# Performance work log

Hardware: AMD Instinct MI355X
Metric: run time of the kernel (lower is better)

The kernel has to match this reference:

```python
import jax, jax.numpy as jnp
import numpy as np

B, N, E = 64, 64, 512          # batch, objects per image, edges per image
OBJ_DIM, Q_DIM, KS = 2048, 1024, 8
HID = Q_DIM // 2               # 512


def setup_inputs() -> dict:
    key = jax.random.key(0)
    k1, k2, k3, k4, k5, k6 = jax.random.split(key, 6)
    node_feats = jax.random.normal(k1, (B, N, OBJ_DIM), jnp.float32)
    q_feats = jax.random.normal(k2, (B, Q_DIM), jnp.float32)
    # Edges: per-image random (i, j) pairs with self-loops removed, indices into
    # the flattened [B*N*N] pairwise tensor, sorted by batch (m//b per image).
    i = jax.random.randint(k3, (B, E), 0, N)
    off = jax.random.randint(k4, (B, E), 1, N)
    j = (i + off) % N
    base = jnp.arange(B)[:, None] * (N * N)
    indexes = (base + i * N + j).reshape(-1).astype(jnp.int32)  # [B*E]
    scale = 0.02
    W_obj = jax.random.normal(k5, (OBJ_DIM, HID), jnp.float32) * scale
    b_obj = jnp.zeros((HID,), jnp.float32)
    W_q = jax.random.normal(k6, (Q_DIM, HID * KS), jnp.float32) * scale
    b_q = jnp.zeros((HID * KS,), jnp.float32)
    return {"node_feats": node_feats, "q_feats": q_feats, "indexes": indexes,
            "W_obj": W_obj, "b_obj": b_obj, "W_q": W_q, "b_q": b_q}


def reference(node_feats, q_feats, indexes, W_obj, b_obj, W_q, b_q):
    b, n, _ = node_feats.shape
    # obj_prob_l: Linear + ReLU -> [B, N, HID]
    node_h = jax.nn.relu(jnp.einsum('bno,oh->bnh', node_feats, W_obj) + b_obj)
    hid = node_h.shape[-1]
    # node_intersect(method='sum') then gather via graph.indexes:
    # equivalent to gathering (i, j) pairs directly instead of materializing [B*N*N, HID]
    bidx = indexes // (n * n)
    rem = indexes % (n * n)
    src = rem // n
    dst = rem % n
    obj_e = node_h[bidx, src] + node_h[bidx, dst]            # [M, HID]
    # q_prob_l: Linear + ReLU -> [B, HID*KS], viewed as per-edge kernels [M, HID, KS]
    q_h = jax.nn.relu(q_feats @ W_q + b_q)                   # [B, HID*KS]
    ks = q_h.shape[-1] // hid
    q_e = q_h.reshape(b, hid, ks)[bidx]                      # [M, HID, KS]
    # batched (1,HID) @ (HID,KS) dot product, then divide by per-kernel norm
    edge_logit = jnp.einsum('mh,mhk->mk', obj_e, q_e)        # [M, KS]
    edge_logit = edge_logit / jnp.linalg.norm(q_e, axis=1)   # [M, KS]
    return edge_logit
```

## Files before the change

### kernel.cpp

```cpp
#include <hip/hip_runtime.h>
#include <hip/hip_bf16.h>


using bf16x8 = __attribute__((ext_vector_type(8))) __bf16;
using f32x4  = __attribute__((ext_vector_type(4))) float;

__device__ __forceinline__ unsigned short f2bf(float f) {
    unsigned int u = __float_as_uint(f);
    unsigned int r = (u + 0x7FFFu + ((u >> 16) & 1u)) >> 16;
    return (unsigned short)r;
}

__device__ __forceinline__ uint4 pk8u(f32x4 a, f32x4 b) {
    union { unsigned short us[8]; uint4 u4; } r;
    r.us[0] = f2bf(a[0]); r.us[1] = f2bf(a[1]); r.us[2] = f2bf(a[2]); r.us[3] = f2bf(a[3]);
    r.us[4] = f2bf(b[0]); r.us[5] = f2bf(b[1]); r.us[6] = f2bf(b[2]); r.us[7] = f2bf(b[3]);
    return r.u4;
}

__device__ __forceinline__ bf16x8 pk8(f32x4 a, f32x4 b) {
    union { uint4 u4; bf16x8 v; } r;
    r.u4 = pk8u(a, b);
    return r.v;
}

__device__ __forceinline__ void gl_lds16(const void* g, void* l) {
    __builtin_amdgcn_global_load_lds(
        (const __attribute__((address_space(1))) unsigned int*)g,
        (__attribute__((address_space(3))) unsigned int*)l,
        16, 0, 0);
}

__global__ __launch_bounds__(256) void cvt_k(const float* __restrict__ nf,
                                             const float* __restrict__ W,
                                             unsigned short* __restrict__ A,
                                             unsigned short* __restrict__ WT) {
    __shared__ float lds[32][33];
    int bid = blockIdx.x;
    if (bid < 2048) {
        int tid = bid * 256 + threadIdx.x;
        for (int p = tid; p < 1048576; p += 524288) {
            int r = p >> 8;
            int grp = p & 255;
            int chunk = grp >> 3, slot = grp & 7;
            int sslot = slot ^ (r & 7);
            const float* src = nf + (size_t)r * 2048 + chunk * 64 + sslot * 8;
            f32x4 v0 = *(const f32x4*)(src);
            f32x4 v1 = *(const f32x4*)(src + 4);
            *(uint4*)(A + (size_t)r * 2048 + chunk * 64 + slot * 8) = pk8u(v0, v1);
        }
    } else {
        int g = bid - 2048;
        int k0 = (g & 63) * 32, n0 = (g >> 6) * 32;
        int tx = threadIdx.x & 31, ty = threadIdx.x >> 5;
#pragma unroll
        for (int j = 0; j < 4; ++j)
            lds[ty + j * 8][tx] = W[(size_t)(k0 + ty + j * 8) * 512 + n0 + tx];
        __syncthreads();
#pragma unroll
        for (int j = 0; j < 4; ++j) {
            int n = n0 + ty + j * 8;
            int k = k0 + tx;
            int chunk = k >> 6, off = k & 63;
            int ksw = chunk * 64 + (((off >> 3) ^ (n & 7)) << 3) + (k & 7);
            WT[(size_t)n * 2048 + ksw] = f2bf(lds[tx][ty + j * 8]);
        }
    }
}

__device__ __forceinline__ void gemm1_body(char* smem, int g1, int t,
                                           const unsigned short* __restrict__ A,
                                           const unsigned short* __restrict__ BT,
                                           const float* __restrict__ bias,
                                           float* __restrict__ C) {
    unsigned short* AsmB = (unsigned short*)smem;
    unsigned short* BsmB = (unsigned short*)(smem + 16384);

    int swz = (g1 & 7) * 64 + (g1 >> 3);
    int by = swz >> 3, bx = swz & 7;
    int m0 = by * 64, n0 = bx * 64;

    int lane = t & 63, w = t >> 6;
    int wm = w >> 1, wn = w & 1;
    int l15 = lane & 15, l16 = lane >> 4;

    const unsigned short* aG = A  + (size_t)(m0 + w * 16 + (lane >> 3)) * 2048 + (lane & 7) * 8;
    const unsigned short* bG = BT + (size_t)(n0 + w * 16 + (lane >> 3)) * 2048 + (lane & 7) * 8;

    f32x4 acc[2][2];
#pragma unroll
    for (int i = 0; i < 2; ++i)
#pragma unroll
        for (int j = 0; j < 2; ++j) acc[i][j] = (f32x4){0.f, 0.f, 0.f, 0.f};

#define G1_STAGE(buf, step)                                                    \
    do {                                                                       \
        int _ko = (step) * 64;                                                 \
        unsigned short* _aL = AsmB + (buf) * 4096 + (w * 16) * 64;             \
        unsigned short* _bL = BsmB + (buf) * 4096 + (w * 16) * 64;             \
        gl_lds16(aG + _ko, _aL);                                               \
        gl_lds16(aG + (size_t)8 * 2048 + _ko, _aL + 512);                      \
        gl_lds16(bG + _ko, _bL);                                               \
        gl_lds16(bG + (size_t)8 * 2048 + _ko, _bL + 512);                      \
    } while (0)

    G1_STAGE(0, 0);
    __syncthreads();

    for (int s = 0; s < 32; ++s) {
        int cur = s & 1;
        if (s < 31) G1_STAGE(cur ^ 1, s + 1);

        const char* Ab = (const char*)(AsmB + cur * 4096);
        const char* Bb = (const char*)(BsmB + cur * 4096);
        int r0 = wm * 32 + l15, r1 = r0 + 16;
        int c0n = wn * 32 + l15, c1n = c0n + 16;
#pragma unroll
        for (int ks = 0; ks < 2; ++ks) {
            int sx = ((ks * 4 + l16) ^ (l15 & 7)) << 4;
            bf16x8 a0 = *(const bf16x8*)(Ab + r0 * 128 + sx);
            bf16x8 a1 = *(const bf16x8*)(Ab + r1 * 128 + sx);
            bf16x8 b0 = *(const bf16x8*)(Bb + c0n * 128 + sx);
            bf16x8 b1 = *(const bf16x8*)(Bb + c1n * 128 + sx);
            acc[0][0] = __builtin_amdgcn_mfma_f32_16x16x32_bf16(a0, b0, acc[0][0], 0, 0, 0);
            acc[0][1] = __builtin_amdgcn_mfma_f32_16x16x32_bf16(a0, b1, acc[0][1], 0, 0, 0);
            acc[1][0] = __builtin_amdgcn_mfma_f32_16x16x32_bf16(a1, b0, acc[1][0], 0, 0, 0);
            acc[1][1] = __builtin_amdgcn_mfma_f32_16x16x32_bf16(a1, b1, acc[1][1], 0, 0, 0);
        }
        __syncthreads();
    }
#undef G1_STAGE

#pragma unroll
    for (int fm = 0; fm < 2; ++fm)
#pragma unroll
        for (int fn = 0; fn < 2; ++fn) {
            int col = n0 + wn * 32 + fn * 16 + l15;
            float bv = bias[col];
#pragma unroll
            for (int j = 0; j < 4; ++j) {
                int row = m0 + wm * 32 + fm * 16 + l16 * 4 + j;
                float v = acc[fm][fn][j] + bv;
                C[(size_t)row * 512 + col] = v > 0.f ? v : 0.f;
            }
        }
}

#define LDK2 136
__device__ __forceinline__ void gemm2_body(char* smem, int bid2, int t,
                                           const float* __restrict__ qf,
                                           const float* __restrict__ Wq,
                                           float* __restrict__ part) {
    auto Asm = reinterpret_cast<unsigned short(*)[LDK2]>(smem);
    auto Bsm = reinterpret_cast<unsigned short(*)[LDK2]>(smem + 64 * LDK2 * 2);

    int lane = t & 63, w = t >> 6;
    int l15 = lane & 15, l16 = lane >> 4;
    int c0 = (bid2 & 63) * 64;
    int k0 = (bid2 >> 6) * 128;

#pragma unroll
    for (int j = 0; j < 4; ++j) {
        int g = t + j * 256;
        int row = g >> 4, kc = g & 15;
        const float* src = qf + (size_t)row * 1024 + k0 + kc * 8;
        f32x4 v0 = *(const f32x4*)(src);
        f32x4 v1 = *(const f32x4*)(src + 4);
        *(uint4*)(&Asm[row][kc * 8]) = pk8u(v0, v1);
    }
    {
        int kg = t >> 4, cg = t & 15;
        f32x4 wv[8];
#pragma unroll
        for (int kk = 0; kk < 8; ++kk)
            wv[kk] = *(const f32x4*)(Wq + (size_t)(k0 + kg * 8 + kk) * 4096 + c0 + cg * 4);
#pragma unroll
        for (int cc = 0; cc < 4; ++cc) {
            union { unsigned short us[8]; uint4 u4; } p;
#pragma unroll
            for (int kk = 0; kk < 8; ++kk) p.us[kk] = f2bf(wv[kk][cc]);
            *(uint4*)(&Bsm[cg * 4 + cc][kg * 8]) = p.u4;
        }
    }
    __syncthreads();

    f32x4 acc[4];
#pragma unroll
    for (int i = 0; i < 4; ++i) acc[i] = (f32x4){0.f, 0.f, 0.f, 0.f};

#pragma unroll
    for (int ks = 0; ks < 4; ++ks) {
        bf16x8 bfr = *(const bf16x8*)(&Bsm[w * 16 + l15][ks * 32 + l16 * 8]);
#pragma unroll
        for (int i = 0; i < 4; ++i) {
            bf16x8 afr = *(const bf16x8*)(&Asm[i * 16 + l15][ks * 32 + l16 * 8]);
            acc[i] = __builtin_amdgcn_mfma_f32_16x16x32_bf16(afr, bfr, acc[i], 0, 0, 0);
        }
    }

    float* pz = part + (size_t)(bid2 >> 6) * 262144;
    int col = c0 + w * 16 + l15;
#pragma unroll
    for (int i = 0; i < 4; ++i)
#pragma unroll
        for (int j = 0; j < 4; ++j) {
            int row = i * 16 + l16 * 4 + j;
            pz[(size_t)row * 4096 + col] = acc[i][j];
        }
}

__global__ __launch_bounds__(256) void gemm_fused(const unsigned short* A,
                                                  const unsigned short* BT,
                                                  const float* bias, float* C,
                                                  const float* qf, const float* Wq,
                                                  float* part) {
    __shared__ __align__(16) char smem[34816];
    int bid = blockIdx.x, t = threadIdx.x;
    if (bid < 512) gemm1_body(smem, bid, t, A, BT, bias, C);
    else           gemm2_body(smem, bid - 512, t, qf, Wq, part);
}
__global__ __launch_bounds__(256) void gemm1_only(const unsigned short* A,
                                                  const unsigned short* BT,
                                                  const float* bias, float* C) {
    __shared__ __align__(16) char smem[34816];
    gemm1_body(smem, blockIdx.x, threadIdx.x, A, BT, bias, C);
}
__global__ __launch_bounds__(256) void gemm2_only(const float* qf, const float* Wq,
                                                  float* part) {
    __shared__ __align__(16) char smem[34816];
    gemm2_body(smem, blockIdx.x, threadIdx.x, qf, Wq, part);
}

__global__ __launch_bounds__(256) void tail_k(const float* __restrict__ part,
                                              const float* __restrict__ bq,
                                              const float* __restrict__ node_h,
                                              const int* __restrict__ idxs,
                                              float* __restrict__ out) {
    __shared__ float qs[4096];
    __shared__ float red[4][8];
    __shared__ float inv[8];
    __shared__ float Pl[64][8];

    int b = blockIdx.x, t = threadIdx.x;
    int lane = t & 63, w = t >> 6;
    int l15 = lane & 15, l16 = lane >> 4;

#pragma unroll
    for (int j = 0; j < 4; ++j) {
        int c = j * 1024 + t * 4;
        f32x4 a = (f32x4){0.f, 0.f, 0.f, 0.f};
#pragma unroll
        for (int z = 0; z < 8; ++z)
            a += *(const f32x4*)(part + (size_t)z * 262144 + (size_t)b * 4096 + c);
        f32x4 bb = *(const f32x4*)(bq + c);
#pragma unroll
        for (int i = 0; i < 4; ++i) {
            float v = a[i] + bb[i];
            a[i] = v > 0.f ? v : 0.f;
        }
        *(f32x4*)(&qs[c]) = a;
    }
    __syncthreads();

    {
        const float* row = qs + t * 16;
        float sq[8] = {0.f, 0.f, 0.f, 0.f, 0.f, 0.f, 0.f, 0.f};
#pragma unroll
        for (int j = 0; j < 4; ++j) {
            f32x4 v = *(const f32x4*)(row + j * 4);
            sq[(j * 4 + 0) & 7] += v[0] * v[0];
            sq[(j * 4 + 1) & 7] += v[1] * v[1];
            sq[(j * 4 + 2) & 7] += v[2] * v[2];
            sq[(j * 4 + 3) & 7] += v[3] * v[3];
        }
#pragma unroll
        for (int k = 0; k < 8; ++k) {
            float v = sq[k];
            v += __shfl_xor(v, 1);  v += __shfl_xor(v, 2);  v += __shfl_xor(v, 4);
            v += __shfl_xor(v, 8);  v += __shfl_xor(v, 16); v += __shfl_xor(v, 32);
            sq[k] = v;
        }
        if (lane == 0) {
#pragma unroll
            for (int k = 0; k < 8; ++k) red[w][k] = sq[k];
        }
    }
    __syncthreads();
    if (t < 8) {
        float s = red[0][t] + red[1][t] + red[2][t] + red[3][t];
        inv[t] = 1.0f / sqrtf(s);
    }
    __syncthreads();

    {
        bool active = l15 < 8;
        float invv = active ? inv[l15] : 0.f;
        const float* arow = node_h + (size_t)(b * 64 + w * 16 + l15) * 512 + l16 * 8;
        f32x4 acc = (f32x4){0.f, 0.f, 0.f, 0.f};
#pragma unroll
        for (int kt = 0; kt < 16; ++kt) {
            f32x4 v0 = *(const f32x4*)(arow + kt * 32);
            f32x4 v1 = *(const f32x4*)(arow + kt * 32 + 4);
            bf16x8 af = pk8(v0, v1);
            union { unsigned short us[8]; bf16x8 v; } bqf;
#pragma unroll
            for (int i = 0; i < 8; ++i)
                bqf.us[i] = active ? f2bf(qs[kt * 256 + (l16 * 8 + i) * 8 + l15]) : 0;
            acc = __builtin_amdgcn_mfma_f32_16x16x32_bf16(af, bqf.v, acc, 0, 0, 0);
        }
        if (active) {
#pragma unroll
            for (int j = 0; j < 4; ++j)
                Pl[w * 16 + l16 * 4 + j][l15] = acc[j] * invv;
        }
    }
    __syncthreads();

#pragma unroll
    for (int e = 0; e < 2; ++e) {
        int m = b * 512 + e * 256 + t;
        int idx = idxs[m];
        int r = idx & 4095;
        int src = r >> 6, dst = r & 63;
        f32x4 o0 = *(const f32x4*)(&Pl[src][0]) + *(const f32x4*)(&Pl[dst][0]);
        f32x4 o1 = *(const f32x4*)(&Pl[src][4]) + *(const f32x4*)(&Pl[dst][4]);
        *(f32x4*)(out + (size_t)m * 8)     = o0;
        *(f32x4*)(out + (size_t)m * 8 + 4) = o1;
    }
}

extern "C" void kernel_launch(void* const* d_in, const int* in_sizes, int n_in,
                              void* d_out, int out_size, void* d_ws, size_t ws_size,
                              hipStream_t stream) {
    const float* node_feats = (const float*)d_in[0];
    const float* q_feats    = (const float*)d_in[1];
    const int*   indexes    = (const int*)d_in[2];
    const float* W_obj      = (const float*)d_in[3];
    const float* b_obj      = (const float*)d_in[4];
    const float* W_q        = (const float*)d_in[5];
    const float* b_q        = (const float*)d_in[6];
    float* out = (float*)d_out;

    char* ws = (char*)d_ws;
    unsigned short* A_swz = (unsigned short*)(ws + 0);
    unsigned short* W_T   = (unsigned short*)(ws + 16777216);
    float* node_h         = (float*)(ws + 18874368);

    if (ws_size >= 35651584ull) {
        float* part = (float*)(ws + 27262976);
        cvt_k<<<3072, 256, 0, stream>>>(node_feats, W_obj, A_swz, W_T);
        gemm_fused<<<1024, 256, 0, stream>>>(A_swz, W_T, b_obj, node_h,
                                             q_feats, W_q, part);
        tail_k<<<64, 256, 0, stream>>>(part, b_q, node_h, indexes, out);
    } else {
        float* part = (float*)(ws + 0);
        cvt_k<<<3072, 256, 0, stream>>>(node_feats, W_obj, A_swz, W_T);
        gemm1_only<<<512, 256, 0, stream>>>(A_swz, W_T, b_obj, node_h);
        gemm2_only<<<512, 256, 0, stream>>>(q_feats, W_q, part);
        tail_k<<<64, 256, 0, stream>>>(part, b_q, node_h, indexes, out);
    }
}
```

Baseline: 45.65 us.

## Move q-projection GEMM into conversion kernel and use single-wave 64x64 gemm1 tiles

Runs the q_feats @ W_q partial GEMM blocks inside the bf16 conversion kernel instead of the node GEMM launch, so that work overlaps with the memory-bound conversion. The node GEMM becomes a 64-thread, single-wave kernel where each wave computes a full 64x64 tile with a 4x4 MFMA fragment grid. It replaces block barriers with explicit vmcnt waits on direct-to-LDS loads. This trades fewer threads per CU, and so less latency hiding, for more register reuse per wave and no block-level synchronization.

```diff
diff --git a/kernel.cpp b/kernel.cpp
--- a/kernel.cpp
+++ b/kernel.cpp
@@ -31,14 +31,85 @@
         16, 0, 0);
 }
 
-__global__ __launch_bounds__(256) void cvt_k(const float* __restrict__ nf,
+#define LDK2 136
+__device__ __forceinline__ void gemm2_body(char* smem, int bid2, int t,
+                                           const float* __restrict__ qf,
+                                           const float* __restrict__ Wq,
+                                           float* __restrict__ part) {
+    auto Asm = reinterpret_cast<unsigned short(*)[LDK2]>(smem);
+    auto Bsm = reinterpret_cast<unsigned short(*)[LDK2]>(smem + 64 * LDK2 * 2);
+
+    int lane = t & 63, w = t >> 6;
+    int l15 = lane & 15, l16 = lane >> 4;
+    int c0 = (bid2 & 63) * 64;
+    int k0 = (bid2 >> 6) * 128;
+
+#pragma unroll
+    for (int j = 0; j < 4; ++j) {
+        int g = t + j * 256;
+        int row = g >> 4, kc = g & 15;
+        const float* src = qf + (size_t)row * 1024 + k0 + kc * 8;
+        f32x4 v0 = *(const f32x4*)(src);
+        f32x4 v1 = *(const f32x4*)(src + 4);
+        *(uint4*)(&Asm[row][kc * 8]) = pk8u(v0, v1);
+    }
+    {
+        int kg = t >> 4, cg = t & 15;
+        f32x4 wv[8];
+#pragma unroll
+        for (int kk = 0; kk < 8; ++kk)
+            wv[kk] = *(const f32x4*)(Wq + (size_t)(k0 + kg * 8 + kk) * 4096 + c0 + cg * 4);
+#pragma unroll
+        for (int cc = 0; cc < 4; ++cc) {
+            union { unsigned short us[8]; uint4 u4; } p;
+#pragma unroll
+            for (int kk = 0; kk < 8; ++kk) p.us[kk] = f2bf(wv[kk][cc]);
+            *(uint4*)(&Bsm[cg * 4 + cc][kg * 8]) = p.u4;
+        }
+    }
+    __syncthreads();
+
+    f32x4 acc[4];
+#pragma unroll
+    for (int i = 0; i < 4; ++i) acc[i] = (f32x4){0.f, 0.f, 0.f, 0.f};
+
+#pragma unroll
+    for (int ks = 0; ks < 4; ++ks) {
+        bf16x8 bfr = *(const bf16x8*)(&Bsm[w * 16 + l15][ks * 32 + l16 * 8]);
+#pragma unroll
+        for (int i = 0; i < 4; ++i) {
+            bf16x8 afr = *(const bf16x8*)(&Asm[i * 16 + l15][ks * 32 + l16 * 8]);
+            acc[i] = __builtin_amdgcn_mfma_f32_16x16x32_bf16(afr, bfr, acc[i], 0, 0, 0);
+        }
+    }
+
+    float* pz = part + (size_t)(bid2 >> 6) * 262144;
+    int col = c0 + w * 16 + l15;
+#pragma unroll
+    for (int i = 0; i < 4; ++i)
+#pragma unroll
+        for (int j = 0; j < 4; ++j) {
+            int row = i * 16 + l16 * 4 + j;
+            pz[(size_t)row * 4096 + col] = acc[i][j];
+        }
+}
+
+__global__ __launch_bounds__(256) void pre_k(const float* __restrict__ nf,
                                              const float* __restrict__ W,
                                              unsigned short* __restrict__ A,
-                                             unsigned short* __restrict__ WT) {
-    __shared__ float lds[32][33];
-    int bid = blockIdx.x;
-    if (bid < 2048) {
-        int tid = bid * 256 + threadIdx.x;
+                                             unsigned short* __restrict__ WT,
+                                             const float* __restrict__ qf,
+                                             const float* __restrict__ Wq,
+                                             float* __restrict__ part, int g2n) {
+    __shared__ __align__(16) char smem[34816];
+    int bid = blockIdx.x, t = threadIdx.x;
+    if (bid < g2n) {
+        gemm2_body(smem, bid, t, qf, Wq, part);
+        return;
+    }
+    int cb = bid - g2n;
+    if (cb < 2048) {
+        int tid = cb * 256 + t;
         for (int p = tid; p < 1048576; p += 524288) {
             int r = p >> 8;
             int grp = p & 255;
@@ -50,9 +121,10 @@
             *(uint4*)(A + (size_t)r * 2048 + chunk * 64 + slot * 8) = pk8u(v0, v1);
         }
     } else {
-        int g = bid - 2048;
+        auto lds = reinterpret_cast<float(*)[33]>(smem);
+        int g = cb - 2048;
         int k0 = (g & 63) * 32, n0 = (g >> 6) * 32;
-        int tx = threadIdx.x & 31, ty = threadIdx.x >> 5;
+        int tx = t & 31, ty = t >> 5;
 #pragma unroll
         for (int j = 0; j < 4; ++j)
             lds[ty + j * 8][tx] = W[(size_t)(k0 + ty + j * 8) * 512 + n0 + tx];
@@ -68,163 +140,89 @@
     }
 }
 
-__device__ __forceinline__ void gemm1_body(char* smem, int g1, int t,
-                                           const unsigned short* __restrict__ A,
-                                           const unsigned short* __restrict__ BT,
-                                           const float* __restrict__ bias,
-                                           float* __restrict__ C) {
-    unsigned short* AsmB = (unsigned short*)smem;
-    unsigned short* BsmB = (unsigned short*)(smem + 16384);
-
-    int swz = (g1 & 7) * 64 + (g1 >> 3);
-    int by = swz >> 3, bx = swz & 7;
-    int m0 = by * 64, n0 = bx * 64;
-
-    int lane = t & 63, w = t >> 6;
-    int wm = w >> 1, wn = w & 1;
+__global__ __launch_bounds__(64) void gemm1(const unsigned short* __restrict__ A,
+                                            const unsigned short* __restrict__ BT,
+                                            const float* __restrict__ bias,
+                                            float* __restrict__ C) {
+    __shared__ __align__(16) unsigned short Asm[2][64 * 64];
+    __shared__ __align__(16) unsigned short Bsm[2][64 * 64];
+
+    int bid = blockIdx.x;
+    int swz = (bid & 7) * 64 + (bid >> 3);
+    int m0 = (swz >> 3) * 64, n0 = (swz & 7) * 64;
+
+    int lane = threadIdx.x;
     int l15 = lane & 15, l16 = lane >> 4;
 
-    const unsigned short* aG = A  + (size_t)(m0 + w * 16 + (lane >> 3)) * 2048 + (lane & 7) * 8;
-    const unsigned short* bG = BT + (size_t)(n0 + w * 16 + (lane >> 3)) * 2048 + (lane & 7) * 8;
-
-    f32x4 acc[2][2];
-#pragma unroll
-    for (int i = 0; i < 2; ++i)
-#pragma unroll
-        for (int j = 0; j < 2; ++j) acc[i][j] = (f32x4){0.f, 0.f, 0.f, 0.f};
+    const unsigned short* aG = A  + (size_t)(m0 + (lane >> 3)) * 2048 + (lane & 7) * 8;
+    const unsigned short* bG = BT + (size_t)(n0 + (lane >> 3)) * 2048 + (lane & 7) * 8;
+
+    f32x4 acc[4][4];
+#pragma unroll
+    for (int i = 0; i < 4; ++i)
+#pragma unroll
+        for (int j = 0; j < 4; ++j) acc[i][j] = (f32x4){0.f, 0.f, 0.f, 0.f};
 
 #define G1_STAGE(buf, step)                                                    \
     do {                                                                       \
         int _ko = (step) * 64;                                                 \
-        unsigned short* _aL = AsmB + (buf) * 4096 + (w * 16) * 64;             \
-        unsigned short* _bL = BsmB + (buf) * 4096 + (w * 16) * 64;             \
-        gl_lds16(aG + _ko, _aL);                                               \
-        gl_lds16(aG + (size_t)8 * 2048 + _ko, _aL + 512);                      \
-        gl_lds16(bG + _ko, _bL);                                               \
-        gl_lds16(bG + (size_t)8 * 2048 + _ko, _bL + 512);                      \
+        _Pragma("unroll")                                                      \
+        for (int _i = 0; _i < 8; ++_i)                                         \
+            gl_lds16(aG + (size_t)(_i * 8) * 2048 + _ko, &Asm[buf][_i * 512]); \
+        _Pragma("unroll")                                                      \
+        for (int _i = 0; _i < 8; ++_i)                                         \
+            gl_lds16(bG + (size_t)(_i * 8) * 2048 + _ko, &Bsm[buf][_i * 512]); \
     } while (0)
 
     G1_STAGE(0, 0);
-    __syncthreads();
 
     for (int s = 0; s < 32; ++s) {
         int cur = s & 1;
-        if (s < 31) G1_STAGE(cur ^ 1, s + 1);
-
-        const char* Ab = (const char*)(AsmB + cur * 4096);
-        const char* Bb = (const char*)(BsmB + cur * 4096);
-        int r0 = wm * 32 + l15, r1 = r0 + 16;
-        int c0n = wn * 32 + l15, c1n = c0n + 16;
+        if (s < 31) {
+            G1_STAGE(cur ^ 1, s + 1);
+            asm volatile("s_waitcnt vmcnt(16)" ::: "memory");
+        } else {
+            asm volatile("s_waitcnt vmcnt(0)" ::: "memory");
+        }
+        __builtin_amdgcn_sched_barrier(0);
+
+        const char* Ab = (const char*)Asm[cur];
+        const char* Bb = (const char*)Bsm[cur];
 #pragma unroll
         for (int ks = 0; ks < 2; ++ks) {
             int sx = ((ks * 4 + l16) ^ (l15 & 7)) << 4;
-            bf16x8 a0 = *(const bf16x8*)(Ab + r0 * 128 + sx);
-            bf16x8 a1 = *(const bf16x8*)(Ab + r1 * 128 + sx);
-            bf16x8 b0 = *(const bf16x8*)(Bb + c0n * 128 + sx);
-            bf16x8 b1 = *(const bf16x8*)(Bb + c1n * 128 + sx);
-            acc[0][0] = __builtin_amdgcn_mfma_f32_16x16x32_bf16(a0, b0, acc[0][0], 0, 0, 0);
-            acc[0][1] = __builtin_amdgcn_mfma_f32_16x16x32_bf16(a0, b1, acc[0][1], 0, 0, 0);
-            acc[1][0] = __builtin_amdgcn_mfma_f32_16x16x32_bf16(a1, b0, acc[1][0], 0, 0, 0);
-            acc[1][1] = __builtin_amdgcn_mfma_f32_16x16x32_bf16(a1, b1, acc[1][1], 0, 0, 0);
-        }
-        __syncthreads();
+            bf16x8 af[4], bf[4];
+#pragma unroll
+            for (int fm = 0; fm < 4; ++fm)
+                af[fm] = *(const bf16x8*)(Ab + (fm * 16 + l15) * 128 + sx);
+#pragma unroll
+            for (int fn = 0; fn < 4; ++fn)
+                bf[fn] = *(const bf16x8*)(Bb + (fn * 16 + l15) * 128 + sx);
+#pragma unroll
+            for (int fm = 0; fm < 4; ++fm)
+#pragma unroll
+                for (int fn = 0; fn < 4; ++fn)
+                    acc[fm][fn] = __builtin_amdgcn_mfma_f32_16x16x32_bf16(
+                        af[fm], bf[fn], acc[fm][fn], 0, 0, 0);
+        }
     }
 #undef G1_STAGE
 
 #pragma unroll
-    for (int fm = 0; fm < 2; ++fm)
-#pragma unroll
-        for (int fn = 0; fn < 2; ++fn) {
-            int col = n0 + wn * 32 + fn * 16 + l15;
+    for (int fm = 0; fm < 4; ++fm)
+#pragma unroll
+        for (int fn = 0; fn < 4; ++fn) {
+            int col = n0 + fn * 16 + l15;
             float bv = bias[col];
 #pragma unroll
             for (int j = 0; j < 4; ++j) {
-                int row = m0 + wm * 32 + fm * 16 + l16 * 4 + j;
+                int row = m0 + fm * 16 + l16 * 4 + j;
                 float v = acc[fm][fn][j] + bv;
                 C[(size_t)row * 512 + col] = v > 0.f ? v : 0.f;
             }
         }
 }
 
-#define LDK2 136
-__device__ __forceinline__ void gemm2_body(char* smem, int bid2, int t,
-                                           const float* __restrict__ qf,
-                                           const float* __restrict__ Wq,
-                                           float* __restrict__ part) {
-    auto Asm = reinterpret_cast<unsigned short(*)[LDK2]>(smem);
-    auto Bsm = reinterpret_cast<unsigned short(*)[LDK2]>(smem + 64 * LDK2 * 2);
-
-    int lane = t & 63, w = t >> 6;
-    int l15 = lane & 15, l16 = lane >> 4;
-    int c0 = (bid2 & 63) * 64;
-    int k0 = (bid2 >> 6) * 128;
-
-#pragma unroll
-    for (int j = 0; j < 4; ++j) {
-        int g = t + j * 256;
-        int row = g >> 4, kc = g & 15;
-        const float* src = qf + (size_t)row * 1024 + k0 + kc * 8;
-        f32x4 v0 = *(const f32x4*)(src);
-        f32x4 v1 = *(const f32x4*)(src + 4);
-        *(uint4*)(&Asm[row][kc * 8]) = pk8u(v0, v1);
-    }
-    {
-        int kg = t >> 4, cg = t & 15;
-        f32x4 wv[8];
-#pragma unroll
-        for (int kk = 0; kk < 8; ++kk)
-            wv[kk] = *(const f32x4*)(Wq + (size_t)(k0 + kg * 8 + kk) * 4096 + c0 + cg * 4);
-#pragma unroll
-        for (int cc = 0; cc < 4; ++cc) {
-            union { unsigned short us[8]; uint4 u4; } p;
-#pragma unroll
-            for (int kk = 0; kk < 8; ++kk) p.us[kk] = f2bf(wv[kk][cc]);
-            *(uint4*)(&Bsm[cg * 4 + cc][kg * 8]) = p.u4;
-        }
-    }
-    __syncthreads();
-
-    f32x4 acc[4];
-#pragma unroll
-    for (int i = 0; i < 4; ++i) acc[i] = (f32x4){0.f, 0.f, 0.f, 0.f};
-
-#pragma unroll
-    for (int ks = 0; ks < 4; ++ks) {
-        bf16x8 bfr = *(const bf16x8*)(&Bsm[w * 16 + l15][ks * 32 + l16 * 8]);
-#pragma unroll
-        for (int i = 0; i < 4; ++i) {
-            bf16x8 afr = *(const bf16x8*)(&Asm[i * 16 + l15][ks * 32 + l16 * 8]);
-            acc[i] = __builtin_amdgcn_mfma_f32_16x16x32_bf16(afr, bfr, acc[i], 0, 0, 0);
-        }
-    }
-
-    float* pz = part + (size_t)(bid2 >> 6) * 262144;
-    int col = c0 + w * 16 + l15;
-#pragma unroll
-    for (int i = 0; i < 4; ++i)
-#pragma unroll
-        for (int j = 0; j < 4; ++j) {
-            int row = i * 16 + l16 * 4 + j;
-            pz[(size_t)row * 4096 + col] = acc[i][j];
-        }
-}
-
-__global__ __launch_bounds__(256) void gemm_fused(const unsigned short* A,
-                                                  const unsigned short* BT,
-                                                  const float* bias, float* C,
-                                                  const float* qf, const float* Wq,
-                                                  float* part) {
-    __shared__ __align__(16) char smem[34816];
-    int bid = blockIdx.x, t = threadIdx.x;
-    if (bid < 512) gemm1_body(smem, bid, t, A, BT, bias, C);
-    else           gemm2_body(smem, bid - 512, t, qf, Wq, part);
-}
-__global__ __launch_bounds__(256) void gemm1_only(const unsigned short* A,
-                                                  const unsigned short* BT,
-                                                  const float* bias, float* C) {
-    __shared__ __align__(16) char smem[34816];
-    gemm1_body(smem, blockIdx.x, threadIdx.x, A, BT, bias, C);
-}
 __global__ __launch_bounds__(256) void gemm2_only(const float* qf, const float* Wq,
                                                   float* part) {
     __shared__ __align__(16) char smem[34816];
@@ -348,14 +346,15 @@
 
     if (ws_size >= 35651584ull) {
         float* part = (float*)(ws + 27262976);
-        cvt_k<<<3072, 256, 0, stream>>>(node_feats, W_obj, A_swz, W_T);
-        gemm_fused<<<1024, 256, 0, stream>>>(A_swz, W_T, b_obj, node_h,
-                                             q_feats, W_q, part);
+        pre_k<<<3584, 256, 0, stream>>>(node_feats, W_obj, A_swz, W_T,
+                                        q_feats, W_q, part, 512);
+        gemm1<<<512, 64, 0, stream>>>(A_swz, W_T, b_obj, node_h);
         tail_k<<<64, 256, 0, stream>>>(part, b_q, node_h, indexes, out);
     } else {
         float* part = (float*)(ws + 0);
-        cvt_k<<<3072, 256, 0, stream>>>(node_feats, W_obj, A_swz, W_T);
-        gemm1_only<<<512, 256, 0, stream>>>(A_swz, W_T, b_obj, node_h);
+        pre_k<<<3072, 256, 0, stream>>>(node_feats, W_obj, A_swz, W_T,
+                                        q_feats, W_q, nullptr, 0);
+        gemm1<<<512, 64, 0, stream>>>(A_swz, W_T, b_obj, node_h);
         gemm2_only<<<512, 256, 0, stream>>>(q_feats, W_q, part);
         tail_k<<<64, 256, 0, stream>>>(part, b_q, node_h, indexes, out);
     }
```

New measurement: 61.56 us. 34.9% more time.

## Triple-buffer gemm1 pipeline, widen gemm2 tiles, schedule gemm2 blocks first

Applied to the files above, without the earlier changes.

The node GEMM's K loop moves from double to triple buffering. It uses explicit vmcnt waits so two stages stay in flight, raises wave priority around the MFMA section, and replaces __syncthreads with raw barriers. The q GEMM now computes 128-column tiles per block, which halves its block count to 256. Those blocks are placed first in the fused launch so the fp32-loading work starts early. LDS use grows to about 51KB per block, which may lower occupancy.

```diff
diff --git a/kernel.cpp b/kernel.cpp
--- a/kernel.cpp
+++ b/kernel.cpp
@@ -74,7 +74,7 @@
                                            const float* __restrict__ bias,
                                            float* __restrict__ C) {
     unsigned short* AsmB = (unsigned short*)smem;
-    unsigned short* BsmB = (unsigned short*)(smem + 16384);
+    unsigned short* BsmB = (unsigned short*)(smem + 24576);
 
     int swz = (g1 & 7) * 64 + (g1 >> 3);
     int by = swz >> 3, bx = swz & 7;
@@ -105,16 +105,24 @@
     } while (0)
 
     G1_STAGE(0, 0);
-    __syncthreads();
-
+    G1_STAGE(1, 1);
+    asm volatile("s_waitcnt vmcnt(4)" ::: "memory");
+    __builtin_amdgcn_sched_barrier(0);
+    __builtin_amdgcn_s_barrier();
+    __builtin_amdgcn_sched_barrier(0);
+
+    int buf = 0;
     for (int s = 0; s < 32; ++s) {
-        int cur = s & 1;
-        if (s < 31) G1_STAGE(cur ^ 1, s + 1);
-
-        const char* Ab = (const char*)(AsmB + cur * 4096);
-        const char* Bb = (const char*)(BsmB + cur * 4096);
+        if (s < 30) {
+            int nb = buf + 2; if (nb >= 3) nb -= 3;
+            G1_STAGE(nb, s + 2);
+        }
+
+        const char* Ab = (const char*)(AsmB + buf * 4096);
+        const char* Bb = (const char*)(BsmB + buf * 4096);
         int r0 = wm * 32 + l15, r1 = r0 + 16;
         int c0n = wn * 32 + l15, c1n = c0n + 16;
+        __builtin_amdgcn_s_setprio(1);
 #pragma unroll
         for (int ks = 0; ks < 2; ++ks) {
             int sx = ((ks * 4 + l16) ^ (l15 & 7)) << 4;
@@ -127,7 +135,16 @@
             acc[1][0] = __builtin_amdgcn_mfma_f32_16x16x32_bf16(a1, b0, acc[1][0], 0, 0, 0);
             acc[1][1] = __builtin_amdgcn_mfma_f32_16x16x32_bf16(a1, b1, acc[1][1], 0, 0, 0);
         }
-        __syncthreads();
+        __builtin_amdgcn_s_setprio(0);
+
+        if (s < 31) {
+            if (s < 30) asm volatile("s_waitcnt vmcnt(4)" ::: "memory");
+            else        asm volatile("s_waitcnt vmcnt(0)" ::: "memory");
+            __builtin_amdgcn_sched_barrier(0);
+            __builtin_amdgcn_s_barrier();
+            __builtin_amdgcn_sched_barrier(0);
+        }
+        buf = (buf == 2) ? 0 : buf + 1;
     }
 #undef G1_STAGE
 
@@ -156,8 +173,8 @@
 
     int lane = t & 63, w = t >> 6;
     int l15 = lane & 15, l16 = lane >> 4;
-    int c0 = (bid2 & 63) * 64;
-    int k0 = (bid2 >> 6) * 128;
+    int c0 = (bid2 & 31) * 128;
+    int k0 = (bid2 >> 5) * 128;
 
 #pragma unroll
     for (int j = 0; j < 4; ++j) {
@@ -168,8 +185,10 @@
         f32x4 v1 = *(const f32x4*)(src + 4);
         *(uint4*)(&Asm[row][kc * 8]) = pk8u(v0, v1);
     }
-    {
-        int kg = t >> 4, cg = t & 15;
+#pragma unroll
+    for (int j = 0; j < 2; ++j) {
+        int g = t + j * 256;
+        int kg = g >> 5, cg = g & 31;
         f32x4 wv[8];
 #pragma unroll
         for (int kk = 0; kk < 8; ++kk)
@@ -184,28 +203,37 @@
     }
     __syncthreads();
 
-    f32x4 acc[4];
-#pragma unroll
-    for (int i = 0; i < 4; ++i) acc[i] = (f32x4){0.f, 0.f, 0.f, 0.f};
+    f32x4 acc[4][2];
+#pragma unroll
+    for (int i = 0; i < 4; ++i)
+#pragma unroll
+        for (int j = 0; j < 2; ++j) acc[i][j] = (f32x4){0.f, 0.f, 0.f, 0.f};
 
 #pragma unroll
     for (int ks = 0; ks < 4; ++ks) {
-        bf16x8 bfr = *(const bf16x8*)(&Bsm[w * 16 + l15][ks * 32 + l16 * 8]);
+        bf16x8 bfr[2];
+#pragma unroll
+        for (int jn = 0; jn < 2; ++jn)
+            bfr[jn] = *(const bf16x8*)(&Bsm[w * 32 + jn * 16 + l15][ks * 32 + l16 * 8]);
 #pragma unroll
         for (int i = 0; i < 4; ++i) {
             bf16x8 afr = *(const bf16x8*)(&Asm[i * 16 + l15][ks * 32 + l16 * 8]);
-            acc[i] = __builtin_amdgcn_mfma_f32_16x16x32_bf16(afr, bfr, acc[i], 0, 0, 0);
-        }
-    }
-
-    float* pz = part + (size_t)(bid2 >> 6) * 262144;
-    int col = c0 + w * 16 + l15;
+            acc[i][0] = __builtin_amdgcn_mfma_f32_16x16x32_bf16(afr, bfr[0], acc[i][0], 0, 0, 0);
+            acc[i][1] = __builtin_amdgcn_mfma_f32_16x16x32_bf16(afr, bfr[1], acc[i][1], 0, 0, 0);
+        }
+    }
+
+    float* pz = part + (size_t)(bid2 >> 5) * 262144;
 #pragma unroll
     for (int i = 0; i < 4; ++i)
 #pragma unroll
-        for (int j = 0; j < 4; ++j) {
-            int row = i * 16 + l16 * 4 + j;
-            pz[(size_t)row * 4096 + col] = acc[i][j];
+        for (int jn = 0; jn < 2; ++jn) {
+            int col = c0 + w * 32 + jn * 16 + l15;
+#pragma unroll
+            for (int j = 0; j < 4; ++j) {
+                int row = i * 16 + l16 * 4 + j;
+                pz[(size_t)row * 4096 + col] = acc[i][jn][j];
+            }
         }
 }
 
@@ -214,20 +242,20 @@
                                                   const float* bias, float* C,
                                                   const float* qf, const float* Wq,
                                                   float* part) {
-    __shared__ __align__(16) char smem[34816];
+    __shared__ __align__(16) char smem[52224];
     int bid = blockIdx.x, t = threadIdx.x;
-    if (bid < 512) gemm1_body(smem, bid, t, A, BT, bias, C);
-    else           gemm2_body(smem, bid - 512, t, qf, Wq, part);
+    if (bid < 256) gemm2_body(smem, bid, t, qf, Wq, part);
+    else           gemm1_body(smem, bid - 256, t, A, BT, bias, C);
 }
 __global__ __launch_bounds__(256) void gemm1_only(const unsigned short* A,
                                                   const unsigned short* BT,
                                                   const float* bias, float* C) {
-    __shared__ __align__(16) char smem[34816];
+    __shared__ __align__(16) char smem[52224];
     gemm1_body(smem, blockIdx.x, threadIdx.x, A, BT, bias, C);
 }
 __global__ __launch_bounds__(256) void gemm2_only(const float* qf, const float* Wq,
                                                   float* part) {
-    __shared__ __align__(16) char smem[34816];
+    __shared__ __align__(16) char smem[52224];
     gemm2_body(smem, blockIdx.x, threadIdx.x, qf, Wq, part);
 }
 
@@ -349,14 +377,14 @@
     if (ws_size >= 35651584ull) {
         float* part = (float*)(ws + 27262976);
         cvt_k<<<3072, 256, 0, stream>>>(node_feats, W_obj, A_swz, W_T);
-        gemm_fused<<<1024, 256, 0, stream>>>(A_swz, W_T, b_obj, node_h,
-                                             q_feats, W_q, part);
+        gemm_fused<<<768, 256, 0, stream>>>(A_swz, W_T, b_obj, node_h,
+                                            q_feats, W_q, part);
         tail_k<<<64, 256, 0, stream>>>(part, b_q, node_h, indexes, out);
     } else {
         float* part = (float*)(ws + 0);
         cvt_k<<<3072, 256, 0, stream>>>(node_feats, W_obj, A_swz, W_T);
         gemm1_only<<<512, 256, 0, stream>>>(A_swz, W_T, b_obj, node_h);
-        gemm2_only<<<512, 256, 0, stream>>>(q_feats, W_q, part);
+        gemm2_only<<<256, 256, 0, stream>>>(q_feats, W_q, part);
         tail_k<<<64, 256, 0, stream>>>(part, b_q, node_h, indexes, out);
     }
 }
```

After: 42.76 us. 1.07x faster.
